# Optimization experiments

Measured on AMD Instinct MI355X. Metric: run time of the kernel, lower is better.

The kernel has to match this reference:

```python
import jax, jax.numpy as jnp
import numpy as np

DIM = 1024
NUM_EXPERTS = 8
ACTIVE_EXPERTS = 2
EXPERT_DIM = 2048


def setup_inputs() -> dict:
    key = jax.random.key(0)
    k1, k2, k3, k4 = jax.random.split(key, 4)
    x = jax.random.normal(k1, (1, 2048, DIM), dtype=jnp.float32)
    gate_w = jax.random.normal(k2, (NUM_EXPERTS, DIM), dtype=jnp.float32) * 0.02
    balance_bias = jnp.zeros((NUM_EXPERTS,), dtype=jnp.float32)
    w1 = jax.random.normal(k3, (NUM_EXPERTS, EXPERT_DIM, DIM), dtype=jnp.float32) * 0.02
    w2 = jax.random.normal(k4, (NUM_EXPERTS, DIM, EXPERT_DIM), dtype=jnp.float32) * 0.02
    return {"x": x, "gate_w": gate_w, "balance_bias": balance_bias, "w1": w1, "w2": w2}


def reference(x, gate_w, balance_bias, w1, w2):
    B, S, D = x.shape
    T = B * S
    xf = x.reshape(T, D)
    # gating: sigmoid scores with load-balance bias, then top-k
    gate_logits = jnp.einsum('td,ed->te', xf, gate_w)
    gate_scores = jax.nn.sigmoid(gate_logits + balance_bias)
    topk_scores, topk_idx = jax.lax.top_k(gate_scores, ACTIVE_EXPERTS)
    topk_scores = topk_scores / (topk_scores.sum(axis=-1, keepdims=True) + 1e-6)
    # scatter normalized scores into dense combine weights [T, E]
    comb = jnp.zeros((T, NUM_EXPERTS), dtype=x.dtype)
    comb = comb.at[jnp.arange(T)[:, None], topk_idx].add(topk_scores)
    # expert FFNs (dense over experts; combine weight zeroes unselected)
    h = jax.nn.silu(jnp.einsum('td,ehd->teh', xf, w1))   # [T, E, expert_dim]
    expert_out = jnp.einsum('teh,edh->ted', h, w2)        # [T, E, D]
    out = jnp.einsum('te,ted->td', comb, expert_out)
    return out.reshape(B, S, D)
```

## Files before the change

### kernel.cpp

```cpp
#include <hip/hip_runtime.h>

#define T 2048
#define DIM 1024
#define NE 8
#define ED 2048
#define NSLOT (T * 2)
#define KSPLIT 2
#define WTOT (NE * ED * DIM)
#define CONVBLK (WTOT / 8 / 256)

#define BM 128
#define BN 128
#define BK 32
#define MAXWL 40

typedef __attribute__((ext_vector_type(8))) short s8v;
typedef __attribute__((ext_vector_type(4))) float f32x4;

__device__ __forceinline__ short f2bf(float f) {
    union { float f; unsigned u; } v;
    v.f = f;
    unsigned r = 0x7FFFu + ((v.u >> 16) & 1u);
    v.u += r;
    return (short)(v.u >> 16);
}

__device__ __forceinline__ float bf2f(short s) {
    union { unsigned u; float f; } v;
    v.u = ((unsigned)(unsigned short)s) << 16;
    return v.f;
}

__device__ __forceinline__ void glds16(const void* g, void* l) {
    __builtin_amdgcn_global_load_lds(
        (const __attribute__((address_space(1))) void*)g,
        (__attribute__((address_space(3))) void*)l, 16, 0, 0);
}

__global__ __launch_bounds__(256) void prep_kernel(
    const float* __restrict__ w1, const float* __restrict__ w2,
    short* __restrict__ w1b, short* __restrict__ w2b,
    const float* __restrict__ x, const float* __restrict__ gw,
    const float* __restrict__ bias, short* __restrict__ xb,
    int* __restrict__ counts, int* __restrict__ top2i, float* __restrict__ top2w) {
    int bx = blockIdx.x;
    if (bx < CONVBLK) {
        size_t c = (size_t)bx * 256 + threadIdx.x;
        const float* p1 = w1 + c * 8;
        const float* p2 = w2 + c * 8;
        float4 a0 = *(const float4*)(p1);
        float4 a1 = *(const float4*)(p1 + 4);
        float4 b0 = *(const float4*)(p2);
        float4 b1 = *(const float4*)(p2 + 4);
        s8v o1 = { f2bf(a0.x), f2bf(a0.y), f2bf(a0.z), f2bf(a0.w),
                   f2bf(a1.x), f2bf(a1.y), f2bf(a1.z), f2bf(a1.w) };
        s8v o2 = { f2bf(b0.x), f2bf(b0.y), f2bf(b0.z), f2bf(b0.w),
                   f2bf(b1.x), f2bf(b1.y), f2bf(b1.z), f2bf(b1.w) };
        *(s8v*)(w1b + c * 8) = o1;
        *(s8v*)(w2b + c * 8) = o2;
        return;
    }
    int wid = threadIdx.x >> 6;
    int lane = threadIdx.x & 63;
    int t = (bx - CONVBLK) * 4 + wid;

    const float* xr = x + (size_t)t * DIM + lane * 16;
    float4 xv[4];
#pragma unroll
    for (int j = 0; j < 4; ++j) xv[j] = *(const float4*)(xr + j * 4);

    s8v o0, o1;
#pragma unroll
    for (int j = 0; j < 2; ++j) {
        o0[j * 4 + 0] = f2bf(xv[j].x); o0[j * 4 + 1] = f2bf(xv[j].y);
        o0[j * 4 + 2] = f2bf(xv[j].z); o0[j * 4 + 3] = f2bf(xv[j].w);
        o1[j * 4 + 0] = f2bf(xv[j + 2].x); o1[j * 4 + 1] = f2bf(xv[j + 2].y);
        o1[j * 4 + 2] = f2bf(xv[j + 2].z); o1[j * 4 + 3] = f2bf(xv[j + 2].w);
    }
    *(s8v*)(xb + (size_t)t * DIM + lane * 16) = o0;
    *(s8v*)(xb + (size_t)t * DIM + lane * 16 + 8) = o1;

    float sc[NE];
#pragma unroll
    for (int e = 0; e < NE; ++e) {
        const float* gr = gw + e * DIM + lane * 16;
        float p = 0.f;
#pragma unroll
        for (int j = 0; j < 4; ++j) {
            float4 g = *(const float4*)(gr + j * 4);
            p += xv[j].x * g.x + xv[j].y * g.y + xv[j].z * g.z + xv[j].w * g.w;
        }
#pragma unroll
        for (int off = 32; off; off >>= 1) p += __shfl_xor(p, off, 64);
        sc[e] = 1.f / (1.f + __expf(-(p + bias[e])));
    }
    int b0 = 0; float s0 = sc[0];
#pragma unroll
    for (int e = 1; e < NE; ++e) if (sc[e] > s0) { s0 = sc[e]; b0 = e; }
    int b1 = -1; float s1 = -1e30f;
#pragma unroll
    for (int e = 0; e < NE; ++e) if (e != b0 && sc[e] > s1) { s1 = sc[e]; b1 = e; }
    float inv = 1.f / (s0 + s1 + 1e-6f);
    if (lane == 0) {
        top2i[t * 2 + 0] = b0; top2i[t * 2 + 1] = b1;
        top2w[t * 2 + 0] = s0 * inv; top2w[t * 2 + 1] = s1 * inv;
        atomicAdd(&counts[b0], 1);
        atomicAdd(&counts[b1], 1);
    }
}

__global__ __launch_bounds__(256) void plan_kernel(
    const int* __restrict__ counts, const int* __restrict__ top2i,
    int* __restrict__ offsets, int* __restrict__ tok_list, int* __restrict__ slot_of,
    int* __restrict__ wl, int* __restrict__ nwl) {
    __shared__ int soff[NE];
    __shared__ int srun[NE];
    if (threadIdx.x == 0) {
        int a = 0;
        for (int e = 0; e < NE; ++e) { soff[e] = a; offsets[e] = a; a += counts[e]; srun[e] = 0; }
        int n = 0;
        for (int e = 0; e < NE; ++e) {
            int mt = (counts[e] + BM - 1) / BM;
            for (int m = 0; m < mt; ++m) wl[n++] = (e << 16) | m;
        }
        *nwl = n;
    }
    __syncthreads();
    for (int t = threadIdx.x; t < T; t += 256) {
#pragma unroll
        for (int k = 0; k < 2; ++k) {
            int e = top2i[t * 2 + k];
            int pos = atomicAdd(&srun[e], 1);
            int slot = soff[e] + pos;
            tok_list[slot] = t;
            slot_of[t * 2 + k] = slot;
        }
    }
}

__global__ __launch_bounds__(256) void ffn1_kernel(
    const short* __restrict__ xb, const short* __restrict__ w1b,
    const int* __restrict__ counts, const int* __restrict__ offsets,
    const int* __restrict__ tok_list, const int* __restrict__ wl,
    const int* __restrict__ nwl, short* __restrict__ h) {
    int my = blockIdx.y;
    if (my >= *nwl) return;
    int e = wl[my] >> 16;
    int m0 = (wl[my] & 0xffff) * BM;
    int cnt = counts[e];
    int off = offsets[e];
    int n0 = blockIdx.x * BN;

    __shared__ __align__(16) short As[2][4][BM][8];
    __shared__ __align__(16) short Bs[2][4][BN][8];

    int tid = threadIdx.x;
    int lane = tid & 63, w = tid >> 6;
    int mo = (w >> 1) * 64, no = (w & 1) * 64;
    int lrow = lane & 15, lq = lane >> 4;

    f32x4 acc[4][4];
#pragma unroll
    for (int mi = 0; mi < 4; ++mi)
#pragma unroll
        for (int ni = 0; ni < 4; ++ni) acc[mi][ni] = (f32x4){0.f, 0.f, 0.f, 0.f};

    int ra0 = m0 + lane;      if (ra0 > cnt - 1) ra0 = cnt - 1;
    int ra1 = m0 + 64 + lane; if (ra1 > cnt - 1) ra1 = cnt - 1;
    const short* a0 = xb + (size_t)tok_list[off + ra0] * DIM + w * 8;
    const short* a1 = xb + (size_t)tok_list[off + ra1] * DIM + w * 8;
    const short* b0 = w1b + ((size_t)e * ED + n0 + lane) * DIM + w * 8;
    const short* b1 = b0 + (size_t)64 * DIM;
    short* lA0 = &As[0][w][0][0];
    short* lA1 = &As[0][w][64][0];
    short* lB0 = &Bs[0][w][0][0];
    short* lB1 = &Bs[0][w][64][0];
    const int BUFO = 4 * BM * 8;

    const int NK = DIM / BK;
    glds16(a0, lA0); glds16(a1, lA1); glds16(b0, lB0); glds16(b1, lB1);

    for (int kk = 0; kk < NK; ++kk) {
        int cur = kk & 1;
        __syncthreads();
        if (kk + 1 < NK) {
            int nb = (cur ^ 1) * BUFO;
            int k0 = (kk + 1) * BK;
            glds16(a0 + k0, lA0 + nb);
            glds16(a1 + k0, lA1 + nb);
            glds16(b0 + k0, lB0 + nb);
            glds16(b1 + k0, lB1 + nb);
        }
        s8v af[4], bf[4];
#pragma unroll
        for (int mi = 0; mi < 4; ++mi) af[mi] = *(const s8v*)&As[cur][lq][mo + mi * 16 + lrow][0];
#pragma unroll
        for (int ni = 0; ni < 4; ++ni) bf[ni] = *(const s8v*)&Bs[cur][lq][no + ni * 16 + lrow][0];
#pragma unroll
        for (int mi = 0; mi < 4; ++mi)
#pragma unroll
            for (int ni = 0; ni < 4; ++ni)
                acc[mi][ni] = __builtin_amdgcn_mfma_f32_16x16x32_bf16(af[mi], bf[ni], acc[mi][ni], 0, 0, 0);
    }

#pragma unroll
    for (int mi = 0; mi < 4; ++mi) {
#pragma unroll
        for (int ni = 0; ni < 4; ++ni) {
            int ln = n0 + no + ni * 16 + lrow;
#pragma unroll
            for (int r = 0; r < 4; ++r) {
                int row = m0 + mo + mi * 16 + lq * 4 + r;
                if (row < cnt) {
                    float v = acc[mi][ni][r];
                    v = v / (1.f + __expf(-v));
                    h[(size_t)(off + row) * ED + ln] = f2bf(v);
                }
            }
        }
    }
}

__global__ __launch_bounds__(256) void ffn2_kernel(
    const short* __restrict__ h, const short* __restrict__ w2b,
    const int* __restrict__ counts, const int* __restrict__ offsets,
    const int* __restrict__ wl, const int* __restrict__ nwl,
    short* __restrict__ eo) {
    int my = blockIdx.y;
    if (my >= *nwl) return;
    int e = wl[my] >> 16;
    int m0 = (wl[my] & 0xffff) * BM;
    int ks = blockIdx.z;
    int cnt = counts[e];
    int off = offsets[e];
    int n0 = blockIdx.x * BN;
    const int kbase = ks * (ED / KSPLIT);

    __shared__ __align__(16) short As[2][4][BM][8];
    __shared__ __align__(16) short Bs[2][4][BN][8];

    int tid = threadIdx.x;
    int lane = tid & 63, w = tid >> 6;
    int mo = (w >> 1) * 64, no = (w & 1) * 64;
    int lrow = lane & 15, lq = lane >> 4;

    f32x4 acc[4][4];
#pragma unroll
    for (int mi = 0; mi < 4; ++mi)
#pragma unroll
        for (int ni = 0; ni < 4; ++ni) acc[mi][ni] = (f32x4){0.f, 0.f, 0.f, 0.f};

    int ra0 = m0 + lane;      if (ra0 > cnt - 1) ra0 = cnt - 1;
    int ra1 = m0 + 64 + lane; if (ra1 > cnt - 1) ra1 = cnt - 1;
    const short* a0 = h + (size_t)(off + ra0) * ED + kbase + w * 8;
    const short* a1 = h + (size_t)(off + ra1) * ED + kbase + w * 8;
    const short* b0 = w2b + ((size_t)e * DIM + n0 + lane) * ED + kbase + w * 8;
    const short* b1 = b0 + (size_t)64 * ED;
    short* lA0 = &As[0][w][0][0];
    short* lA1 = &As[0][w][64][0];
    short* lB0 = &Bs[0][w][0][0];
    short* lB1 = &Bs[0][w][64][0];
    const int BUFO = 4 * BM * 8;

    const int NK = (ED / KSPLIT) / BK;
    glds16(a0, lA0); glds16(a1, lA1); glds16(b0, lB0); glds16(b1, lB1);

    for (int kk = 0; kk < NK; ++kk) {
        int cur = kk & 1;
        __syncthreads();
        if (kk + 1 < NK) {
            int nb = (cur ^ 1) * BUFO;
            int k0 = (kk + 1) * BK;
            glds16(a0 + k0, lA0 + nb);
            glds16(a1 + k0, lA1 + nb);
            glds16(b0 + k0, lB0 + nb);
            glds16(b1 + k0, lB1 + nb);
        }
        s8v af[4], bf[4];
#pragma unroll
        for (int mi = 0; mi < 4; ++mi) af[mi] = *(const s8v*)&As[cur][lq][mo + mi * 16 + lrow][0];
#pragma unroll
        for (int ni = 0; ni < 4; ++ni) bf[ni] = *(const s8v*)&Bs[cur][lq][no + ni * 16 + lrow][0];
#pragma unroll
        for (int mi = 0; mi < 4; ++mi)
#pragma unroll
            for (int ni = 0; ni < 4; ++ni)
                acc[mi][ni] = __builtin_amdgcn_mfma_f32_16x16x32_bf16(af[mi], bf[ni], acc[mi][ni], 0, 0, 0);
    }

    short* eop = eo + (size_t)ks * NSLOT * DIM;
#pragma unroll
    for (int mi = 0; mi < 4; ++mi) {
#pragma unroll
        for (int ni = 0; ni < 4; ++ni) {
            int ln = n0 + no + ni * 16 + lrow;
#pragma unroll
            for (int r = 0; r < 4; ++r) {
                int row = m0 + mo + mi * 16 + lq * 4 + r;
                if (row < cnt) {
                    eop[(size_t)(off + row) * DIM + ln] = f2bf(acc[mi][ni][r]);
                }
            }
        }
    }
}

__global__ __launch_bounds__(256) void combine_kernel(
    const short* __restrict__ eo, const int* __restrict__ slot_of,
    const float* __restrict__ top2w, float* __restrict__ out) {
    int idx = blockIdx.x * 256 + threadIdx.x;
    int t = idx >> 7;
    int c = idx & 127;
    int s0 = slot_of[2 * t], s1 = slot_of[2 * t + 1];
    float w0 = top2w[2 * t], w1 = top2w[2 * t + 1];
    const short* e0 = eo;
    const short* e1 = eo + (size_t)NSLOT * DIM;
    s8v a0 = *(const s8v*)(e0 + (size_t)s0 * DIM + c * 8);
    s8v a1 = *(const s8v*)(e1 + (size_t)s0 * DIM + c * 8);
    s8v b0 = *(const s8v*)(e0 + (size_t)s1 * DIM + c * 8);
    s8v b1 = *(const s8v*)(e1 + (size_t)s1 * DIM + c * 8);
    float4 o[2];
#pragma unroll
    for (int j = 0; j < 8; ++j) {
        float v = w0 * (bf2f(a0[j]) + bf2f(a1[j])) + w1 * (bf2f(b0[j]) + bf2f(b1[j]));
        ((float*)o)[j] = v;
    }
    float4* op = (float4*)(out + (size_t)t * DIM + c * 8);
    op[0] = o[0];
    op[1] = o[1];
}

extern "C" void kernel_launch(void* const* d_in, const int* in_sizes, int n_in,
                              void* d_out, int out_size, void* d_ws, size_t ws_size,
                              hipStream_t stream) {
    const float* x    = (const float*)d_in[0];
    const float* gw   = (const float*)d_in[1];
    const float* bias = (const float*)d_in[2];
    const float* w1   = (const float*)d_in[3];
    const float* w2   = (const float*)d_in[4];
    float* out = (float*)d_out;

    char* ws = (char*)d_ws;
    short* xb  = (short*)ws;
    short* h   = (short*)(ws + (4ull << 20));
    short* w1b = (short*)(ws + (20ull << 20));
    short* eo  = (short*)(ws + (20ull << 20));
    short* w2b = (short*)(ws + (52ull << 20));
    char* meta = ws + (84ull << 20);
    int*   counts   = (int*)(meta);
    int*   offsets  = (int*)(meta + 64);
    int*   tok_list = (int*)(meta + 128);
    int*   slot_of  = (int*)(meta + 128 + 4 * NSLOT);
    int*   top2i    = (int*)(meta + 128 + 8 * NSLOT);
    float* top2w    = (float*)(meta + 128 + 8 * NSLOT + 8 * T);
    int*   wl       = (int*)(meta + 128 + 8 * NSLOT + 16 * T);
    int*   nwl      = (int*)(meta + 128 + 8 * NSLOT + 16 * T + 4 * MAXWL);

    hipMemsetAsync(counts, 0, 32, stream);

    prep_kernel<<<CONVBLK + T / 4, 256, 0, stream>>>(w1, w2, w1b, w2b,
                                                     x, gw, bias, xb, counts, top2i, top2w);
    plan_kernel<<<1, 256, 0, stream>>>(counts, top2i, offsets, tok_list, slot_of, wl, nwl);
    ffn1_kernel<<<dim3(ED / BN, MAXWL), 256, 0, stream>>>(xb, w1b, counts, offsets, tok_list, wl, nwl, h);
    ffn2_kernel<<<dim3(DIM / BN, MAXWL, KSPLIT), 256, 0, stream>>>(h, w2b, counts, offsets, wl, nwl, eo);
    combine_kernel<<<T * DIM / 8 / 256, 256, 0, stream>>>(eo, slot_of, top2w, out);
}
```

Baseline: 326.5 us.

## Fuse fp32-to-bf16 weight conversion into expert GEMM tile loads

```diff
diff --git a/kernel.cpp b/kernel.cpp
--- a/kernel.cpp
+++ b/kernel.cpp
@@ -6,8 +6,6 @@
 #define ED 2048
 #define NSLOT (T * 2)
 #define KSPLIT 2
-#define WTOT (NE * ED * DIM)
-#define CONVBLK (WTOT / 8 / 256)
 
 #define BM 128
 #define BN 128
@@ -31,38 +29,28 @@
     return v.f;
 }
 
+__device__ __forceinline__ unsigned pkbf2(float lo, float hi) {
+    union { float f; unsigned u; } a, b;
+    a.f = lo; b.f = hi;
+    return __builtin_amdgcn_perm(b.u + 0x8000u, a.u + 0x8000u, 0x07060302u);
+}
+
 __device__ __forceinline__ void glds16(const void* g, void* l) {
     __builtin_amdgcn_global_load_lds(
         (const __attribute__((address_space(1))) void*)g,
         (__attribute__((address_space(3))) void*)l, 16, 0, 0);
 }
 
-__global__ __launch_bounds__(256) void prep_kernel(
-    const float* __restrict__ w1, const float* __restrict__ w2,
-    short* __restrict__ w1b, short* __restrict__ w2b,
-    const float* __restrict__ x, const float* __restrict__ gw,
-    const float* __restrict__ bias, short* __restrict__ xb,
-    int* __restrict__ counts, int* __restrict__ top2i, float* __restrict__ top2w) {
-    int bx = blockIdx.x;
-    if (bx < CONVBLK) {
-        size_t c = (size_t)bx * 256 + threadIdx.x;
-        const float* p1 = w1 + c * 8;
-        const float* p2 = w2 + c * 8;
-        float4 a0 = *(const float4*)(p1);
-        float4 a1 = *(const float4*)(p1 + 4);
-        float4 b0 = *(const float4*)(p2);
-        float4 b1 = *(const float4*)(p2 + 4);
-        s8v o1 = { f2bf(a0.x), f2bf(a0.y), f2bf(a0.z), f2bf(a0.w),
-                   f2bf(a1.x), f2bf(a1.y), f2bf(a1.z), f2bf(a1.w) };
-        s8v o2 = { f2bf(b0.x), f2bf(b0.y), f2bf(b0.z), f2bf(b0.w),
-                   f2bf(b1.x), f2bf(b1.y), f2bf(b1.z), f2bf(b1.w) };
-        *(s8v*)(w1b + c * 8) = o1;
-        *(s8v*)(w2b + c * 8) = o2;
-        return;
-    }
+__global__ void router_kernel(const float* __restrict__ x,
+                              const float* __restrict__ gw,
+                              const float* __restrict__ bias,
+                              short* __restrict__ xb,
+                              int* __restrict__ counts,
+                              int* __restrict__ top2i,
+                              float* __restrict__ top2w) {
     int wid = threadIdx.x >> 6;
     int lane = threadIdx.x & 63;
-    int t = (bx - CONVBLK) * 4 + wid;
+    int t = blockIdx.x * 4 + wid;
 
     const float* xr = x + (size_t)t * DIM + lane * 16;
     float4 xv[4];
@@ -139,7 +127,7 @@
 }
 
 __global__ __launch_bounds__(256) void ffn1_kernel(
-    const short* __restrict__ xb, const short* __restrict__ w1b,
+    const short* __restrict__ xb, const float* __restrict__ w1,
     const int* __restrict__ counts, const int* __restrict__ offsets,
     const int* __restrict__ tok_list, const int* __restrict__ wl,
     const int* __restrict__ nwl, short* __restrict__ h) {
@@ -152,7 +140,7 @@
     int n0 = blockIdx.x * BN;
 
     __shared__ __align__(16) short As[2][4][BM][8];
-    __shared__ __align__(16) short Bs[2][4][BN][8];
+    __shared__ __align__(16) short Bs[4][BN][8];
 
     int tid = threadIdx.x;
     int lane = tid & 63, w = tid >> 6;
@@ -169,33 +157,38 @@
     int ra1 = m0 + 64 + lane; if (ra1 > cnt - 1) ra1 = cnt - 1;
     const short* a0 = xb + (size_t)tok_list[off + ra0] * DIM + w * 8;
     const short* a1 = xb + (size_t)tok_list[off + ra1] * DIM + w * 8;
-    const short* b0 = w1b + ((size_t)e * ED + n0 + lane) * DIM + w * 8;
-    const short* b1 = b0 + (size_t)64 * DIM;
-    short* lA0 = &As[0][w][0][0];
-    short* lA1 = &As[0][w][64][0];
-    short* lB0 = &Bs[0][w][0][0];
-    short* lB1 = &Bs[0][w][64][0];
-    const int BUFO = 4 * BM * 8;
+
+    int br = tid >> 1, bq = tid & 1;
+    const float* bp = w1 + ((size_t)e * ED + n0 + br) * DIM + bq * 16;
 
     const int NK = DIM / BK;
-    glds16(a0, lA0); glds16(a1, lA1); glds16(b0, lB0); glds16(b1, lB1);
+    float4 L0, L1, L2, L3;
+    L0 = *(const float4*)(bp);     L1 = *(const float4*)(bp + 4);
+    L2 = *(const float4*)(bp + 8); L3 = *(const float4*)(bp + 12);
+    glds16(a0, &As[0][w][0][0]);
+    glds16(a1, &As[0][w][64][0]);
 
     for (int kk = 0; kk < NK; ++kk) {
         int cur = kk & 1;
         __syncthreads();
+        uint4 p0 = { pkbf2(L0.x, L0.y), pkbf2(L0.z, L0.w), pkbf2(L1.x, L1.y), pkbf2(L1.z, L1.w) };
+        uint4 p1 = { pkbf2(L2.x, L2.y), pkbf2(L2.z, L2.w), pkbf2(L3.x, L3.y), pkbf2(L3.z, L3.w) };
+        *(uint4*)&Bs[2 * bq][br][0] = p0;
+        *(uint4*)&Bs[2 * bq + 1][br][0] = p1;
+        __syncthreads();
         if (kk + 1 < NK) {
-            int nb = (cur ^ 1) * BUFO;
             int k0 = (kk + 1) * BK;
-            glds16(a0 + k0, lA0 + nb);
-            glds16(a1 + k0, lA1 + nb);
-            glds16(b0 + k0, lB0 + nb);
-            glds16(b1 + k0, lB1 + nb);
+            glds16(a0 + k0, &As[cur ^ 1][w][0][0]);
+            glds16(a1 + k0, &As[cur ^ 1][w][64][0]);
+            const float* bpp = bp + k0;
+            L0 = *(const float4*)(bpp);     L1 = *(const float4*)(bpp + 4);
+            L2 = *(const float4*)(bpp + 8); L3 = *(const float4*)(bpp + 12);
         }
         s8v af[4], bf[4];
 #pragma unroll
         for (int mi = 0; mi < 4; ++mi) af[mi] = *(const s8v*)&As[cur][lq][mo + mi * 16 + lrow][0];
 #pragma unroll
-        for (int ni = 0; ni < 4; ++ni) bf[ni] = *(const s8v*)&Bs[cur][lq][no + ni * 16 + lrow][0];
+        for (int ni = 0; ni < 4; ++ni) bf[ni] = *(const s8v*)&Bs[lq][no + ni * 16 + lrow][0];
 #pragma unroll
         for (int mi = 0; mi < 4; ++mi)
 #pragma unroll
@@ -222,7 +215,7 @@
 }
 
 __global__ __launch_bounds__(256) void ffn2_kernel(
-    const short* __restrict__ h, const short* __restrict__ w2b,
+    const short* __restrict__ h, const float* __restrict__ w2,
     const int* __restrict__ counts, const int* __restrict__ offsets,
     const int* __restrict__ wl, const int* __restrict__ nwl,
     short* __restrict__ eo) {
@@ -230,14 +223,14 @@
     if (my >= *nwl) return;
     int e = wl[my] >> 16;
     int m0 = (wl[my] & 0xffff) * BM;
-    int ks = blockIdx.z;
+    int ksp = blockIdx.z;
     int cnt = counts[e];
     int off = offsets[e];
     int n0 = blockIdx.x * BN;
-    const int kbase = ks * (ED / KSPLIT);
+    const int kbase = ksp * (ED / KSPLIT);
 
     __shared__ __align__(16) short As[2][4][BM][8];
-    __shared__ __align__(16) short Bs[2][4][BN][8];
+    __shared__ __align__(16) short Bs[4][BN][8];
 
     int tid = threadIdx.x;
     int lane = tid & 63, w = tid >> 6;
@@ -254,33 +247,38 @@
     int ra1 = m0 + 64 + lane; if (ra1 > cnt - 1) ra1 = cnt - 1;
     const short* a0 = h + (size_t)(off + ra0) * ED + kbase + w * 8;
     const short* a1 = h + (size_t)(off + ra1) * ED + kbase + w * 8;
-    const short* b0 = w2b + ((size_t)e * DIM + n0 + lane) * ED + kbase + w * 8;
-    const short* b1 = b0 + (size_t)64 * ED;
-    short* lA0 = &As[0][w][0][0];
-    short* lA1 = &As[0][w][64][0];
-    short* lB0 = &Bs[0][w][0][0];
-    short* lB1 = &Bs[0][w][64][0];
-    const int BUFO = 4 * BM * 8;
+
+    int br = tid >> 1, bq = tid & 1;
+    const float* bp = w2 + ((size_t)e * DIM + n0 + br) * ED + kbase + bq * 16;
 
     const int NK = (ED / KSPLIT) / BK;
-    glds16(a0, lA0); glds16(a1, lA1); glds16(b0, lB0); glds16(b1, lB1);
+    float4 L0, L1, L2, L3;
+    L0 = *(const float4*)(bp);     L1 = *(const float4*)(bp + 4);
+    L2 = *(const float4*)(bp + 8); L3 = *(const float4*)(bp + 12);
+    glds16(a0, &As[0][w][0][0]);
+    glds16(a1, &As[0][w][64][0]);
 
     for (int kk = 0; kk < NK; ++kk) {
         int cur = kk & 1;
         __syncthreads();
+        uint4 p0 = { pkbf2(L0.x, L0.y), pkbf2(L0.z, L0.w), pkbf2(L1.x, L1.y), pkbf2(L1.z, L1.w) };
+        uint4 p1 = { pkbf2(L2.x, L2.y), pkbf2(L2.z, L2.w), pkbf2(L3.x, L3.y), pkbf2(L3.z, L3.w) };
+        *(uint4*)&Bs[2 * bq][br][0] = p0;
+        *(uint4*)&Bs[2 * bq + 1][br][0] = p1;
+        __syncthreads();
         if (kk + 1 < NK) {
-            int nb = (cur ^ 1) * BUFO;
             int k0 = (kk + 1) * BK;
-            glds16(a0 + k0, lA0 + nb);
-            glds16(a1 + k0, lA1 + nb);
-            glds16(b0 + k0, lB0 + nb);
-            glds16(b1 + k0, lB1 + nb);
+            glds16(a0 + k0, &As[cur ^ 1][w][0][0]);
+            glds16(a1 + k0, &As[cur ^ 1][w][64][0]);
+            const float* bpp = bp + k0;
+            L0 = *(const float4*)(bpp);     L1 = *(const float4*)(bpp + 4);
+            L2 = *(const float4*)(bpp + 8); L3 = *(const float4*)(bpp + 12);
         }
         s8v af[4], bf[4];
 #pragma unroll
         for (int mi = 0; mi < 4; ++mi) af[mi] = *(const s8v*)&As[cur][lq][mo + mi * 16 + lrow][0];
 #pragma unroll
-        for (int ni = 0; ni < 4; ++ni) bf[ni] = *(const s8v*)&Bs[cur][lq][no + ni * 16 + lrow][0];
+        for (int ni = 0; ni < 4; ++ni) bf[ni] = *(const s8v*)&Bs[lq][no + ni * 16 + lrow][0];
 #pragma unroll
         for (int mi = 0; mi < 4; ++mi)
 #pragma unroll
@@ -288,7 +286,7 @@
                 acc[mi][ni] = __builtin_amdgcn_mfma_f32_16x16x32_bf16(af[mi], bf[ni], acc[mi][ni], 0, 0, 0);
     }
 
-    short* eop = eo + (size_t)ks * NSLOT * DIM;
+    short* eop = eo + (size_t)ksp * NSLOT * DIM;
 #pragma unroll
     for (int mi = 0; mi < 4; ++mi) {
 #pragma unroll
@@ -341,12 +339,10 @@
     float* out = (float*)d_out;
 
     char* ws = (char*)d_ws;
-    short* xb  = (short*)ws;
-    short* h   = (short*)(ws + (4ull << 20));
-    short* w1b = (short*)(ws + (20ull << 20));
-    short* eo  = (short*)(ws + (20ull << 20));
-    short* w2b = (short*)(ws + (52ull << 20));
-    char* meta = ws + (84ull << 20);
+    short* xb = (short*)ws;
+    short* h  = (short*)(ws + (4ull << 20));
+    short* eo = (short*)(ws + (20ull << 20));
+    char* meta = ws + (36ull << 20);
     int*   counts   = (int*)(meta);
     int*   offsets  = (int*)(meta + 64);
     int*   tok_list = (int*)(meta + 128);
@@ -358,10 +354,9 @@
 
     hipMemsetAsync(counts, 0, 32, stream);
 
-    prep_kernel<<<CONVBLK + T / 4, 256, 0, stream>>>(w1, w2, w1b, w2b,
-                                                     x, gw, bias, xb, counts, top2i, top2w);
+    router_kernel<<<T / 4, 256, 0, stream>>>(x, gw, bias, xb, counts, top2i, top2w);
     plan_kernel<<<1, 256, 0, stream>>>(counts, top2i, offsets, tok_list, slot_of, wl, nwl);
-    ffn1_kernel<<<dim3(ED / BN, MAXWL), 256, 0, stream>>>(xb, w1b, counts, offsets, tok_list, wl, nwl, h);
-    ffn2_kernel<<<dim3(DIM / BN, MAXWL, KSPLIT), 256, 0, stream>>>(h, w2b, counts, offsets, wl, nwl, eo);
+    ffn1_kernel<<<dim3(ED / BN, MAXWL), 256, 0, stream>>>(xb, w1, counts, offsets, tok_list, wl, nwl, h);
+    ffn2_kernel<<<dim3(DIM / BN, MAXWL, KSPLIT), 256, 0, stream>>>(h, w2, counts, offsets, wl, nwl, eo);
     combine_kernel<<<T * DIM / 8 / 256, 256, 0, stream>>>(eo, slot_of, top2w, out);
 }
```

Result: no change. 320.5 us (-1.8%).
